# Optimization experiments

Hardware: AMD Instinct MI355X
Metric: run time of the kernel (lower is better)

Reference implementation:

```python
import jax, jax.numpy as jnp
import numpy as np
from jax import lax

K = 7            # cfg.network.PSROI_BINS == pool_size
FEAT_STRIDE = 16
LAMDA = 0.1
D_PER_BIN = 8    # feature channels per position-sensitive bin -> C = K*K*8 = 392


def _bilinear(feat, y, x, extra_idx):
    """Bilinearly sample feat[H,W,...] at float coords (y,x); extra_idx are
    integer index arrays (broadcast to y.shape) selecting trailing feat axes."""
    H, W = feat.shape[0], feat.shape[1]
    y0f = jnp.floor(y); x0f = jnp.floor(x)
    wy = (y - y0f)[..., None]
    wx = (x - x0f)[..., None]
    y0 = jnp.clip(y0f.astype(jnp.int32), 0, H - 1)
    y1 = jnp.clip(y0f.astype(jnp.int32) + 1, 0, H - 1)
    x0 = jnp.clip(x0f.astype(jnp.int32), 0, W - 1)
    x1 = jnp.clip(x0f.astype(jnp.int32) + 1, 0, W - 1)
    def g(yi, xi):
        return feat[(yi, xi) + extra_idx]
    return ((1 - wy) * (1 - wx) * g(y0, x0) + (1 - wy) * wx * g(y0, x1)
            + wy * (1 - wx) * g(y1, x0) + wy * wx * g(y1, x1))


def ps_roi(f, rois, k, feat_stride, offsets=None):
    """Position-sensitive RoI pooling. f: [H,W,C] with C = k*k*D (bin-major
    channel layout). rois: [N,5] (batch, x1, y1, x2, y2) in image coords.
    offsets (optional): [N, k*k, G, 2] per-bin, per-channel-group (x,y) shifts
    in image coords. Returns [N, D, k, k]."""
    H, W, C = f.shape
    N = rois.shape[0]
    kk = k * k
    D = C // kk
    x1 = rois[:, 1] / feat_stride
    y1 = rois[:, 2] / feat_stride
    x2 = (rois[:, 3] + 1.0) / feat_stride
    y2 = (rois[:, 4] + 1.0) / feat_stride
    bw = (x2 - x1) / k  # [N]
    bh = (y2 - y1) / k
    jj = jnp.tile(jnp.arange(k, dtype=f.dtype), k)     # bin = i*k + j
    ii = jnp.repeat(jnp.arange(k, dtype=f.dtype), k)
    cx = x1[:, None] + (jj + 0.5) * bw[:, None]        # [N, kk] bin centers
    cy = y1[:, None] + (ii + 0.5) * bh[:, None]
    bins = jnp.arange(kk, dtype=jnp.int32)
    if offsets is None:
        feat = f.reshape(H, W, kk, D)
        b = jnp.broadcast_to(bins, (N, kk))
        vals = _bilinear(feat, cy, cx, (b,))           # [N, kk, D]
    else:
        G = offsets.shape[2]
        cxg = cx[:, :, None] + offsets[..., 0] / feat_stride  # [N, kk, G]
        cyg = cy[:, :, None] + offsets[..., 1] / feat_stride
        feat = f.reshape(H, W, kk, G, D // G)
        b = jnp.broadcast_to(bins[None, :, None], (N, kk, G))
        g = jnp.broadcast_to(jnp.arange(G, dtype=jnp.int32)[None, None, :], (N, kk, G))
        vals = _bilinear(feat, cyg, cxg, (b, g))       # [N, kk, G, D//G]
        vals = vals.reshape(N, kk, D)
    return jnp.transpose(vals.reshape(N, k, k, D), (0, 3, 1, 2))  # [N, D, k, k]


def setup_inputs():
    key = jax.random.key(0)
    kf, kw, k1, k2 = jax.random.split(key, 4)
    H = W = 128
    C = K * K * D_PER_BIN
    N = 2048
    features = jax.random.normal(kf, (1, H, W, C), jnp.float32)
    conv_w = jax.random.normal(kw, (3, 3, C, 2 * 4 * K * K), jnp.float32) * 0.01
    img = float(H * FEAT_STRIDE)
    xy1 = jax.random.uniform(k1, (N, 2), minval=0.0, maxval=img * 0.6)
    wh = jax.random.uniform(k2, (N, 2), minval=32.0, maxval=img * 0.4)
    xy2 = jnp.minimum(xy1 + wh, img - 1.0)
    rois = jnp.concatenate([jnp.zeros((N, 1)), xy1[:, :1], xy1[:, 1:], xy2[:, :1], xy2[:, 1:]], axis=1).astype(jnp.float32)
    return {"features": features, "rois": rois, "conv_w": conv_w}


def reference(features, rois, conv_w):
    # offset branch: 3x3 conv (no bias) -> PS-RoI pool -> scale by lamda*roi size
    offset_map = lax.conv_general_dilated(features, conv_w, (1, 1), 'SAME',
                                          dimension_numbers=('NHWC', 'HWIO', 'NHWC'))
    off = ps_roi(offset_map[0], rois, K, FEAT_STRIDE)          # [N, 8, K, K]
    N = off.shape[0]
    off = off.reshape(N, -1, 2, K, K)                          # [N, 4, 2, K, K]
    off = jnp.transpose(off, (2, 3, 4, 1, 0))                  # [2, K, K, 4, N]
    roi_w = rois[:, 3] - rois[:, 1] + 1.0
    roi_h = rois[:, 4] - rois[:, 2] + 1.0
    off = jnp.stack((off[0] * roi_w * LAMDA, off[1] * roi_h * LAMDA), axis=0)
    off = jnp.transpose(off, (4, 1, 2, 3, 0))                  # [N, K, K, 4, 2]
    off = off.reshape(N, K * K, -1, 2)                         # [N, kk, 4, 2]
    # deformable PS-RoI pooling of the features with predicted offsets
    return ps_roi(features[0], rois, K, FEAT_STRIDE, offsets=off)  # [N, 8, K, K]
```

## Files before the change

### kernel.cpp

```cpp
#include <hip/hip_runtime.h>
#include <hip/hip_cooperative_groups.h>
#include <cstddef>
#include <cstdint>

namespace cg = cooperative_groups;

#define HH    128
#define WW    128
#define CC    392
#define NPIX  (HH*WW)
#define NROI  2048
#define PSK   7
#define NBIN  49
#define LAMDA 0.1f

#define CPAD      448
#define HPAD      130
#define NPADCO    416
#define SEGSTRIDE (9*CPAD)
#define BKK       64
#define NSS       21
#define SSPLIT    10

#define AROWS   136
#define ATH     (AROWS*BKK)
#define BTH     (128*BKK)

#define NBLK    1024
#define NTHR    256
#define GSTRIDE (NBLK*NTHR)
#define FTOT    (HPAD*HPAD*(CPAD/8))
#define WTILES  (9*14*13)
#define POOL8   (NROI*NBIN*8)

typedef _Float16 half8   __attribute__((ext_vector_type(8)));
typedef _Float16 half2v  __attribute__((ext_vector_type(2)));
typedef float    floatx4 __attribute__((ext_vector_type(4)));

__device__ __forceinline__ void async_ld16(const _Float16* g, _Float16* l) {
  __builtin_amdgcn_global_load_lds((const __attribute__((address_space(1))) void*)g,
                                   (__attribute__((address_space(3))) void*)l,
                                   16, 0, 0);
}

__device__ __forceinline__ void prep_features(const float* __restrict__ F,
                                              _Float16* __restrict__ Fh,
                                              int gtid, int stride) {
  for (int idx = gtid; idx < FTOT; idx += stride) {
    const int p   = idx / (CPAD / 8);
    const int cgi = idx - p * (CPAD / 8);
    const int c   = cgi * 8;
    const int py  = p / HPAD;
    const int px  = p - py * HPAD;
    half8 h;
#pragma unroll
    for (int i = 0; i < 8; ++i) h[i] = (_Float16)0.f;
    if (py >= 1 && py <= HH && px >= 1 && px <= WW && c < CC) {
      const float* src = F + ((size_t)(py - 1) * WW + (px - 1)) * CC + c;
      const float4 v0 = *(const float4*)src;
      const float4 v1 = *(const float4*)(src + 4);
      h[0] = (_Float16)v0.x; h[1] = (_Float16)v0.y;
      h[2] = (_Float16)v0.z; h[3] = (_Float16)v0.w;
      h[4] = (_Float16)v1.x; h[5] = (_Float16)v1.y;
      h[6] = (_Float16)v1.z; h[7] = (_Float16)v1.w;
    }
    *(half8*)(Fh + (size_t)p * CPAD + c) = h;
  }
}

__device__ __forceinline__ void prep_weights(const float* __restrict__ Wt,
                                             _Float16* __restrict__ Bth,
                                             float (*tile)[33],
                                             int bid, int t, int nblocks) {
  for (int tl = bid; tl < WTILES; tl += nblocks) {
    const int seg = tl / (14 * 13);
    const int rem = tl - seg * (14 * 13);
    const int cit = rem / 13;
    const int cot = rem - cit * 13;
    const int ci0 = cit * 32, co0 = cot * 32;
    __syncthreads();
#pragma unroll
    for (int i = 0; i < 4; ++i) {
      const int idx = t + i * 256;
      const int lr = idx >> 5;
      const int lc = idx & 31;
      const int ci = ci0 + lr, co = co0 + lc;
      float v = 0.f;
      if (ci < CC && co < CC) v = Wt[((size_t)seg * CC + ci) * CC + co];
      tile[lr][lc] = v;
    }
    __syncthreads();
#pragma unroll
    for (int i = 0; i < 4; ++i) {
      const int idx = t + i * 256;
      const int lr = idx >> 5;
      const int lc = idx & 31;
      Bth[(size_t)(co0 + lr) * SEGSTRIDE + seg * CPAD + ci0 + lc] = (_Float16)tile[lc][lr];
    }
  }
}

__device__ __forceinline__ void stage_a130(const _Float16* __restrict__ Fh,
                                           int fy, int cb, _Float16* As, int t) {
  const int L = t & 63, w = t >> 6;
  const int srow = L >> 3;
  const int kofs = ((L & 7) ^ srow) * 8;
  const _Float16* gA = Fh + (size_t)fy * HPAD * CPAD + kofs + cb;
#pragma unroll
  for (int j = 0; j < 4; ++j) {
    const int r = w * 32 + j * 8 + srow;
    async_ld16(gA + (size_t)r * CPAD, &As[(w * 32 + j * 8) * BKK]);
  }
  if (w == 0) {
    const int r = 128 + srow;
    const int rp = (r <= 129) ? r : 129;
    async_ld16(gA + (size_t)rp * CPAD, &As[128 * BKK]);
  }
}

__device__ __forceinline__ void conv_fat(const _Float16* __restrict__ Fh,
                                         const _Float16* __restrict__ Bth,
                                         _Float16* __restrict__ OMp,
                                         _Float16* As, _Float16* Bs,
                                         int row0, int col0, int s0, int s1, int t) {
  const int L = t & 63;
  const int w = t >> 6;

  const int srow = L >> 3;
  const int kofs = ((L & 7) ^ srow) * 8;
  const int ya = row0 >> 7;
  const int nbase = col0 + w * 32 + srow;

  const int wm = (w >> 1) * 64;
  const int wn = (w & 1) * 64;
  const int fr = L & 15;
  const int quad = L >> 4;

  floatx4 acc[4][4];
#pragma unroll
  for (int i = 0; i < 4; ++i)
#pragma unroll
    for (int j = 0; j < 4; ++j) {
      floatx4 z = {0.f, 0.f, 0.f, 0.f};
      acc[i][j] = z;
    }

  for (int s = s0; s < s1; ++s) {
    const int dyi = s / 7;
    const int it  = s - dyi * 7;
    const int fy  = ya + dyi;
    const int cb  = it * BKK;

    stage_a130(Fh, fy, cb, As, t);

    for (int dxs = 0; dxs < 3; ++dxs) {
      const int seg = dyi * 3 + dxs;
      const _Float16* gB = Bth + (size_t)nbase * SEGSTRIDE + seg * CPAD + kofs + cb;
#pragma unroll
      for (int j = 0; j < 4; ++j)
        async_ld16(gB + (size_t)(j * 8) * SEGSTRIDE, &Bs[(w * 32 + j * 8) * BKK]);
      __syncthreads();

      half8 a0[4], a1[4], b0[4], b1[4];
#pragma unroll
      for (int mt = 0; mt < 4; ++mt) {
        const int row = wm + mt * 16 + fr + dxs;
        const int rk = row & 7;
        a0[mt] = *(const half8*)(&As[row * BKK + ((quad ^ rk) * 8)]);
        a1[mt] = *(const half8*)(&As[row * BKK + (((4 + quad) ^ rk) * 8)]);
      }
#pragma unroll
      for (int nt = 0; nt < 4; ++nt) {
        const int rb = (wn + nt * 16 + fr) * BKK;
        const int rk = fr & 7;
        b0[nt] = *(const half8*)(&Bs[rb + ((quad ^ rk) * 8)]);
        b1[nt] = *(const half8*)(&Bs[rb + (((4 + quad) ^ rk) * 8)]);
      }
#pragma unroll
      for (int mt = 0; mt < 4; ++mt)
#pragma unroll
        for (int nt = 0; nt < 4; ++nt)
          acc[mt][nt] = __builtin_amdgcn_mfma_f32_16x16x32_f16(a0[mt], b0[nt], acc[mt][nt], 0, 0, 0);
#pragma unroll
      for (int mt = 0; mt < 4; ++mt)
#pragma unroll
        for (int nt = 0; nt < 4; ++nt)
          acc[mt][nt] = __builtin_amdgcn_mfma_f32_16x16x32_f16(a1[mt], b1[nt], acc[mt][nt], 0, 0, 0);
      __syncthreads();
    }
  }

#pragma unroll
  for (int mt = 0; mt < 4; ++mt) {
    const int rbase = row0 + wm + mt * 16 + quad * 4;
#pragma unroll
    for (int nt = 0; nt < 4; ++nt) {
      const int col = col0 + wn + nt * 16 + fr;
      if (col < CC) {
#pragma unroll
        for (int r = 0; r < 4; ++r)
          OMp[(size_t)(rbase + r) * CC + col] = (_Float16)acc[mt][nt][r];
      }
    }
  }
}

__device__ __forceinline__ void conv_thin(const _Float16* __restrict__ Fh,
                                          const _Float16* __restrict__ Bth,
                                          _Float16* __restrict__ OMp,
                                          _Float16* As, _Float16* Bs,
                                          int row0, int s0, int s1, int t) {
  const int L = t & 63;
  const int w = t >> 6;

  const int srow = L >> 3;
  const int kofs = ((L & 7) ^ srow) * 8;
  const int ya = row0 >> 7;
  const int nbase = 384 + w * 8 + srow;

  const int wm = w * 32;
  const int fr = L & 15;
  const int quad = L >> 4;

  floatx4 acc[2];
#pragma unroll
  for (int i = 0; i < 2; ++i) {
    floatx4 z = {0.f, 0.f, 0.f, 0.f};
    acc[i] = z;
  }

  for (int s = s0; s < s1; ++s) {
    const int dyi = s / 7;
    const int it  = s - dyi * 7;
    const int fy  = ya + dyi;
    const int cb  = it * BKK;

    stage_a130(Fh, fy, cb, As, t);

    for (int dxs = 0; dxs < 3; ++dxs) {
      const int seg = dyi * 3 + dxs;
      if (w < 2) {
        const _Float16* gB = Bth + (size_t)nbase * SEGSTRIDE + seg * CPAD + kofs + cb;
        async_ld16(gB, &Bs[(w * 8) * BKK]);
      }
      __syncthreads();

      half8 a0[2], a1[2];
#pragma unroll
      for (int mt = 0; mt < 2; ++mt) {
        const int row = wm + mt * 16 + fr + dxs;
        const int rk = row & 7;
        a0[mt] = *(const half8*)(&As[row * BKK + ((quad ^ rk) * 8)]);
        a1[mt] = *(const half8*)(&As[row * BKK + (((4 + quad) ^ rk) * 8)]);
      }
      const int rk = fr & 7;
      const half8 b0 = *(const half8*)(&Bs[fr * BKK + ((quad ^ rk) * 8)]);
      const half8 b1 = *(const half8*)(&Bs[fr * BKK + (((4 + quad) ^ rk) * 8)]);
#pragma unroll
      for (int mt = 0; mt < 2; ++mt)
        acc[mt] = __builtin_amdgcn_mfma_f32_16x16x32_f16(a0[mt], b0, acc[mt], 0, 0, 0);
#pragma unroll
      for (int mt = 0; mt < 2; ++mt)
        acc[mt] = __builtin_amdgcn_mfma_f32_16x16x32_f16(a1[mt], b1, acc[mt], 0, 0, 0);
      __syncthreads();
    }
  }

#pragma unroll
  for (int mt = 0; mt < 2; ++mt) {
    const int rbase = row0 + wm + mt * 16 + quad * 4;
    const int col = 384 + fr;
    if (col < CC) {
#pragma unroll
      for (int r = 0; r < 4; ++r)
        OMp[(size_t)(rbase + r) * CC + col] = (_Float16)acc[mt][r];
    }
  }
}

__device__ __forceinline__ void conv_dispatch(const _Float16* Fh, const _Float16* Bth,
                                              _Float16* OMa, _Float16* OMb,
                                              _Float16* As, _Float16* Bs,
                                              int bid, int t) {
  const int x = bid & 127;
  const int rest = bid >> 7;
  const int kz = (rest < 6) ? (rest / 3) : (rest - 6);
  _Float16* OMp = kz ? OMb : OMa;
  const int s0 = kz ? SSPLIT : 0;
  const int s1 = kz ? NSS : SSPLIT;
  if (rest < 6)
    conv_fat(Fh, Bth, OMp, As, Bs, x * 128, (rest % 3) * 128, s0, s1, t);
  else
    conv_thin(Fh, Bth, OMp, As, Bs, x * 128, s0, s1, t);
}

__device__ __forceinline__ void bilin_setup(float y, float x,
                                            int& iy0, int& iy1, int& ix0, int& ix1,
                                            float& w00, float& w01, float& w10, float& w11) {
  const float y0f = floorf(y), x0f = floorf(x);
  const float wy = y - y0f, wx = x - x0f;
  const int a = (int)y0f, b = (int)x0f;
  iy0 = min(max(a, 0), HH - 1);
  iy1 = min(max(a + 1, 0), HH - 1);
  ix0 = min(max(b, 0), WW - 1);
  ix1 = min(max(b + 1, 0), WW - 1);
  w00 = (1.f - wy) * (1.f - wx);
  w01 = (1.f - wy) * wx;
  w10 = wy * (1.f - wx);
  w11 = wy * wx;
}

__device__ __forceinline__ void pool_item8(const _Float16* __restrict__ Fh,
                                           const float* __restrict__ R,
                                           const _Float16* __restrict__ OMa,
                                           const _Float16* __restrict__ OMb,
                                           float* __restrict__ out, int tid) {
  const int j  = tid & 7;
  const int nb = tid >> 3;
  const int n  = nb / NBIN;
  const int b  = nb - n * NBIN;
  const int bi = b / PSK;
  const int bj = b - bi * PSK;

  const float rx1 = R[n * 5 + 1], ry1 = R[n * 5 + 2];
  const float rx2 = R[n * 5 + 3], ry2 = R[n * 5 + 4];
  const float x1 = rx1 * (1.f / 16.f);
  const float y1 = ry1 * (1.f / 16.f);
  const float x2 = (rx2 + 1.f) * (1.f / 16.f);
  const float y2 = (ry2 + 1.f) * (1.f / 16.f);
  const float bw = (x2 - x1) * (1.f / 7.f);
  const float bh = (y2 - y1) * (1.f / 7.f);
  const float cx = x1 + ((float)bj + 0.5f) * bw;
  const float cy = y1 + ((float)bi + 0.5f) * bh;
  const float sxs = (rx2 - rx1 + 1.f) * (LAMDA / 16.f);
  const float sys = (ry2 - ry1 + 1.f) * (LAMDA / 16.f);

  int iy0, iy1, ix0, ix1;
  float w00, w01, w10, w11;
  bilin_setup(cy, cx, iy0, iy1, ix0, ix1, w00, w01, w10, w11);

  const int c = j & 3;
  const int cyi = (c >> 1) ? iy1 : iy0;
  const int cxi = (c & 1) ? ix1 : ix0;
  const float wq = (c == 0) ? w00 : (c == 1) ? w01 : (c == 2) ? w10 : w11;

  const _Float16* OMp = (j >> 2) ? OMb : OMa;
  const size_t base = (size_t)(cyi * WW + cxi) * CC + (size_t)b * 8;
  const half8 hv = *(const half8*)(OMp + base);

  float o8[8];
#pragma unroll
  for (int i = 0; i < 8; ++i) o8[i] = wq * (float)hv[i];
#pragma unroll
  for (int i = 0; i < 8; ++i) o8[i] += __shfl_xor(o8[i], 1);
#pragma unroll
  for (int i = 0; i < 8; ++i) o8[i] += __shfl_xor(o8[i], 2);
#pragma unroll
  for (int i = 0; i < 8; ++i) o8[i] += __shfl_xor(o8[i], 4);

  const int g = j & 3;
  const float sx = cx + o8[2 * g] * sxs;
  const float sy = cy + o8[2 * g + 1] * sys;

  int jy0, jy1, jx0, jx1;
  float u00, u01, u10, u11;
  bilin_setup(sy, sx, jy0, jy1, jx0, jx1, u00, u01, u10, u11);

  const int  yh = j >> 2;
  const int  jy = yh ? jy1 : jy0;
  const float ua = yh ? u10 : u00;
  const float ub = yh ? u11 : u01;

  const size_t c0 = (size_t)b * 8 + 2 * g;
  const half2v qa = *(const half2v*)(Fh + ((size_t)(jy + 1) * HPAD + (jx0 + 1)) * CPAD + c0);
  const half2v qb = *(const half2v*)(Fh + ((size_t)(jy + 1) * HPAD + (jx1 + 1)) * CPAD + c0);

  float v0 = ua * (float)qa[0] + ub * (float)qb[0];
  float v1 = ua * (float)qa[1] + ub * (float)qb[1];
  v0 += __shfl_xor(v0, 4);
  v1 += __shfl_xor(v1, 4);

  const float vout = yh ? v1 : v0;
  out[((size_t)n * 8 + 2 * g + yh) * NBIN + b] = vout;
}

__global__ __launch_bounds__(NTHR, 4)
void mega_kernel(const float* __restrict__ F, const float* __restrict__ Wt,
                 _Float16* __restrict__ OMa, _Float16* __restrict__ OMb,
                 _Float16* __restrict__ Fh, _Float16* __restrict__ Bth) {
  __shared__ __align__(16) _Float16 smem[ATH + BTH];
  const int bid = blockIdx.x;
  const int t = threadIdx.x;
  cg::grid_group grid = cg::this_grid();

  prep_features(F, Fh, bid * NTHR + t, GSTRIDE);
  prep_weights(Wt, Bth, (float(*)[33])smem, bid, t, NBLK);

  __threadfence();
  grid.sync();

  conv_dispatch(Fh, Bth, OMa, OMb, smem, smem + ATH, bid, t);
}

__global__ __launch_bounds__(256)
void pool_kernel(const _Float16* __restrict__ Fh, const float* __restrict__ R,
                 const _Float16* __restrict__ OMa, const _Float16* __restrict__ OMb,
                 float* __restrict__ out) {
  pool_item8(Fh, R, OMa, OMb, out, blockIdx.x * 256 + threadIdx.x);
}

__global__ __launch_bounds__(256)
void prep_kernel_sa(const float* __restrict__ F, const float* __restrict__ Wt,
                    _Float16* __restrict__ Fh, _Float16* __restrict__ Bth) {
  __shared__ float tile[32][33];
  prep_features(F, Fh, blockIdx.x * 256 + threadIdx.x, gridDim.x * 256);
  prep_weights(Wt, Bth, tile, blockIdx.x, threadIdx.x, gridDim.x);
}

__global__ __launch_bounds__(256, 4)
void conv_kernel_sa(const _Float16* __restrict__ Fh, const _Float16* __restrict__ Bth,
                    _Float16* __restrict__ OMa, _Float16* __restrict__ OMb) {
  __shared__ __align__(16) _Float16 smem[ATH + BTH];
  conv_dispatch(Fh, Bth, OMa, OMb, smem, smem + ATH, blockIdx.x, threadIdx.x);
}

extern "C" void kernel_launch(void* const* d_in, const int* in_sizes, int n_in,
                              void* d_out, int out_size, void* d_ws, size_t ws_size,
                              hipStream_t stream) {
  const float* F  = (const float*)d_in[0];
  const float* R  = (const float*)d_in[1];
  const float* Wt = (const float*)d_in[2];
  float* out = (float*)d_out;

  const size_t omBytes  = (size_t)NPIX * CC * sizeof(_Float16);
  const size_t fhBytes  = (size_t)HPAD * HPAD * CPAD * sizeof(_Float16);

  _Float16* OMa = (_Float16*)d_ws;
  _Float16* OMb = OMa + (size_t)NPIX * CC;
  _Float16* Fh  = (_Float16*)((char*)d_ws + 2 * omBytes);
  _Float16* Bth = (_Float16*)((char*)d_ws + 2 * omBytes + fhBytes);

  int maxBlk = 0;
  hipError_t qerr = hipOccupancyMaxActiveBlocksPerMultiprocessor(&maxBlk, mega_kernel, NTHR, 0);
  bool coopOk = (qerr == hipSuccess && maxBlk >= 4);

  if (coopOk) {
    void* args[] = {(void*)&F, (void*)&Wt, (void*)&OMa, (void*)&OMb,
                    (void*)&Fh, (void*)&Bth};
    hipError_t err = hipLaunchCooperativeKernel((const void*)mega_kernel,
                                                dim3(NBLK), dim3(NTHR),
                                                args, 0, stream);
    if (err != hipSuccess) {
      (void)hipGetLastError();
      coopOk = false;
    }
  }
  if (!coopOk) {
    prep_kernel_sa<<<2048, 256, 0, stream>>>(F, Wt, Fh, Bth);
    conv_kernel_sa<<<NBLK, 256, 0, stream>>>(Fh, Bth, OMa, OMb);
  }

  pool_kernel<<<POOL8 / 256, 256, 0, stream>>>(Fh, R, OMa, OMb, out);
}
```

Before: 150.8 us.

## Drop split-K conv, use 512-thread blocks with double-buffered LDS pipeline

Removes the split-K partition of the 3x3 conv GEMM, which wrote two partial offset maps that the pool kernel had to sum. Each block now covers the full K range with 8 waves and smaller per-wave tiles, and double-buffers A and B in LDS so the next slice's async global->LDS loads overlap the current MFMAs. This halves the offset-map writes and the pool reads. In exchange it doubles LDS use per block and halves the block count, which may lower occupancy, and the cooperative launch now only requires two resident blocks per CU.

```diff
diff --git a/kernel.cpp b/kernel.cpp
--- a/kernel.cpp
+++ b/kernel.cpp
@@ -16,24 +16,23 @@
 
 #define CPAD      448
 #define HPAD      130
-#define NPADCO    416
 #define SEGSTRIDE (9*CPAD)
 #define BKK       64
 #define NSS       21
-#define SSPLIT    10
-
-#define AROWS   136
-#define ATH     (AROWS*BKK)
+#define NZ        63
+
+#define ATH     (136*BKK)
 #define BTH     (128*BKK)
 
-#define NBLK    1024
-#define NTHR    256
+#define NBLK    512
+#define NTHR    512
 #define GSTRIDE (NBLK*NTHR)
 #define FTOT    (HPAD*HPAD*(CPAD/8))
 #define WTILES  (9*14*13)
 #define POOL8   (NROI*NBIN*8)
 
 typedef _Float16 half8   __attribute__((ext_vector_type(8)));
+typedef _Float16 half4v  __attribute__((ext_vector_type(4)));
 typedef _Float16 half2v  __attribute__((ext_vector_type(2)));
 typedef float    floatx4 __attribute__((ext_vector_type(4)));
 
@@ -41,6 +40,12 @@
   __builtin_amdgcn_global_load_lds((const __attribute__((address_space(1))) void*)g,
                                    (__attribute__((address_space(3))) void*)l,
                                    16, 0, 0);
+}
+
+__device__ __forceinline__ void sync_step() {
+  asm volatile("s_waitcnt vmcnt(0)" ::: "memory");
+  __builtin_amdgcn_s_barrier();
+  asm volatile("" ::: "memory");
 }
 
 __device__ __forceinline__ void prep_features(const float* __restrict__ F,
@@ -71,7 +76,7 @@
 __device__ __forceinline__ void prep_weights(const float* __restrict__ Wt,
                                              _Float16* __restrict__ Bth,
                                              float (*tile)[33],
-                                             int bid, int t, int nblocks) {
+                                             int bid, int t, int bdim, int nblocks) {
   for (int tl = bid; tl < WTILES; tl += nblocks) {
     const int seg = tl / (14 * 13);
     const int rem = tl - seg * (14 * 13);
@@ -79,9 +84,7 @@
     const int cot = rem - cit * 13;
     const int ci0 = cit * 32, co0 = cot * 32;
     __syncthreads();
-#pragma unroll
-    for (int i = 0; i < 4; ++i) {
-      const int idx = t + i * 256;
+    for (int idx = t; idx < 1024; idx += bdim) {
       const int lr = idx >> 5;
       const int lc = idx & 31;
       const int ci = ci0 + lr, co = co0 + lc;
@@ -90,9 +93,7 @@
       tile[lr][lc] = v;
     }
     __syncthreads();
-#pragma unroll
-    for (int i = 0; i < 4; ++i) {
-      const int idx = t + i * 256;
+    for (int idx = t; idx < 1024; idx += bdim) {
       const int lr = idx >> 5;
       const int lc = idx & 31;
       Bth[(size_t)(co0 + lr) * SEGSTRIDE + seg * CPAD + ci0 + lc] = (_Float16)tile[lc][lr];
@@ -100,198 +101,189 @@
   }
 }
 
-__device__ __forceinline__ void stage_a130(const _Float16* __restrict__ Fh,
-                                           int fy, int cb, _Float16* As, int t) {
+__device__ __forceinline__ void stage_a8(const _Float16* __restrict__ Fh,
+                                         int fy, int cb, _Float16* As, int t) {
   const int L = t & 63, w = t >> 6;
   const int srow = L >> 3;
   const int kofs = ((L & 7) ^ srow) * 8;
   const _Float16* gA = Fh + (size_t)fy * HPAD * CPAD + kofs + cb;
 #pragma unroll
-  for (int j = 0; j < 4; ++j) {
-    const int r = w * 32 + j * 8 + srow;
-    async_ld16(gA + (size_t)r * CPAD, &As[(w * 32 + j * 8) * BKK]);
-  }
-  if (w == 0) {
-    const int r = 128 + srow;
-    const int rp = (r <= 129) ? r : 129;
+  for (int j = 0; j < 2; ++j) {
+    const int r = w * 16 + j * 8;
+    async_ld16(gA + (size_t)(r + srow) * CPAD, &As[r * BKK]);
+  }
+  if (w == 7) {
+    const int rr = 128 + srow;
+    const int rp = (rr <= 129) ? rr : 129;
     async_ld16(gA + (size_t)rp * CPAD, &As[128 * BKK]);
   }
+}
+
+__device__ __forceinline__ void stage_b8(const _Float16* __restrict__ Bth,
+                                         int col0, int seg, int cb, _Float16* Bs, int t) {
+  const int L = t & 63, w = t >> 6;
+  const int srow = L >> 3;
+  const int kofs = ((L & 7) ^ srow) * 8;
+  const _Float16* gB = Bth + (size_t)(col0 + w * 16 + srow) * SEGSTRIDE + seg * CPAD + kofs + cb;
+#pragma unroll
+  for (int j = 0; j < 2; ++j)
+    async_ld16(gB + (size_t)(j * 8) * SEGSTRIDE, &Bs[(w * 16 + j * 8) * BKK]);
+}
+
+__device__ __forceinline__ void stage_b_thin8(const _Float16* __restrict__ Bth,
+                                              int seg, int cb, _Float16* Bs, int t) {
+  const int L = t & 63, w = t >> 6;
+  if (w >= 2) return;
+  const int srow = L >> 3;
+  const int kofs = ((L & 7) ^ srow) * 8;
+  const _Float16* gB = Bth + (size_t)(384 + w * 8 + srow) * SEGSTRIDE + seg * CPAD + kofs + cb;
+  async_ld16(gB, &Bs[(w * 8) * BKK]);
 }
 
 __device__ __forceinline__ void conv_fat(const _Float16* __restrict__ Fh,
                                          const _Float16* __restrict__ Bth,
-                                         _Float16* __restrict__ OMp,
+                                         _Float16* __restrict__ OM,
                                          _Float16* As, _Float16* Bs,
-                                         int row0, int col0, int s0, int s1, int t) {
+                                         int row0, int col0, int t) {
   const int L = t & 63;
   const int w = t >> 6;
-
-  const int srow = L >> 3;
-  const int kofs = ((L & 7) ^ srow) * 8;
   const int ya = row0 >> 7;
-  const int nbase = col0 + w * 32 + srow;
-
-  const int wm = (w >> 1) * 64;
-  const int wn = (w & 1) * 64;
   const int fr = L & 15;
   const int quad = L >> 4;
-
-  floatx4 acc[4][4];
+  const int wm = (w >> 2) * 64;
+  const int wn = (w & 3) * 32;
+
+  floatx4 acc[4][2];
 #pragma unroll
   for (int i = 0; i < 4; ++i)
 #pragma unroll
-    for (int j = 0; j < 4; ++j) {
+    for (int j = 0; j < 2; ++j) {
       floatx4 z = {0.f, 0.f, 0.f, 0.f};
       acc[i][j] = z;
     }
 
-  for (int s = s0; s < s1; ++s) {
-    const int dyi = s / 7;
-    const int it  = s - dyi * 7;
-    const int fy  = ya + dyi;
-    const int cb  = it * BKK;
-
-    stage_a130(Fh, fy, cb, As, t);
-
-    for (int dxs = 0; dxs < 3; ++dxs) {
-      const int seg = dyi * 3 + dxs;
-      const _Float16* gB = Bth + (size_t)nbase * SEGSTRIDE + seg * CPAD + kofs + cb;
-#pragma unroll
-      for (int j = 0; j < 4; ++j)
-        async_ld16(gB + (size_t)(j * 8) * SEGSTRIDE, &Bs[(w * 32 + j * 8) * BKK]);
-      __syncthreads();
-
-      half8 a0[4], a1[4], b0[4], b1[4];
+  stage_a8(Fh, ya, 0, As, t);
+  stage_b8(Bth, col0, 0, 0, Bs, t);
+  sync_step();
+
+  int pa = 0, pb = 0;
+  for (int z = 0; z < NZ; ++z) {
+    const int dxs = z - (z / 3) * 3;
+    if (z + 1 < NZ) {
+      const int z2 = z + 1;
+      const int s2 = z2 / 3;
+      const int dxs2 = z2 - s2 * 3;
+      const int dyi2 = s2 / 7;
+      const int it2 = s2 - dyi2 * 7;
+      const int cb2 = it2 * BKK;
+      if (dxs2 == 0) stage_a8(Fh, ya + dyi2, cb2, As + (pa ^ 1) * ATH, t);
+      stage_b8(Bth, col0, dyi2 * 3 + dxs2, cb2, Bs + (pb ^ 1) * BTH, t);
+    }
+    const _Float16* Ab = As + pa * ATH;
+    const _Float16* Bb = Bs + pb * BTH;
+#pragma unroll
+    for (int kh = 0; kh < 2; ++kh) {
+      const int q = kh * 4 + quad;
+      half8 av[4], bv[2];
 #pragma unroll
       for (int mt = 0; mt < 4; ++mt) {
         const int row = wm + mt * 16 + fr + dxs;
-        const int rk = row & 7;
-        a0[mt] = *(const half8*)(&As[row * BKK + ((quad ^ rk) * 8)]);
-        a1[mt] = *(const half8*)(&As[row * BKK + (((4 + quad) ^ rk) * 8)]);
+        av[mt] = *(const half8*)(&Ab[row * BKK + ((q ^ (row & 7)) * 8)]);
       }
 #pragma unroll
-      for (int nt = 0; nt < 4; ++nt) {
-        const int rb = (wn + nt * 16 + fr) * BKK;
-        const int rk = fr & 7;
-        b0[nt] = *(const half8*)(&Bs[rb + ((quad ^ rk) * 8)]);
-        b1[nt] = *(const half8*)(&Bs[rb + (((4 + quad) ^ rk) * 8)]);
+      for (int nt = 0; nt < 2; ++nt) {
+        const int rb = wn + nt * 16 + fr;
+        bv[nt] = *(const half8*)(&Bb[rb * BKK + ((q ^ (fr & 7)) * 8)]);
       }
 #pragma unroll
       for (int mt = 0; mt < 4; ++mt)
 #pragma unroll
-        for (int nt = 0; nt < 4; ++nt)
-          acc[mt][nt] = __builtin_amdgcn_mfma_f32_16x16x32_f16(a0[mt], b0[nt], acc[mt][nt], 0, 0, 0);
-#pragma unroll
-      for (int mt = 0; mt < 4; ++mt)
-#pragma unroll
-        for (int nt = 0; nt < 4; ++nt)
-          acc[mt][nt] = __builtin_amdgcn_mfma_f32_16x16x32_f16(a1[mt], b1[nt], acc[mt][nt], 0, 0, 0);
-      __syncthreads();
-    }
+        for (int nt = 0; nt < 2; ++nt)
+          acc[mt][nt] = __builtin_amdgcn_mfma_f32_16x16x32_f16(av[mt], bv[nt], acc[mt][nt], 0, 0, 0);
+    }
+    sync_step();
+    if (dxs == 2) pa ^= 1;
+    pb ^= 1;
   }
 
 #pragma unroll
   for (int mt = 0; mt < 4; ++mt) {
     const int rbase = row0 + wm + mt * 16 + quad * 4;
 #pragma unroll
-    for (int nt = 0; nt < 4; ++nt) {
+    for (int nt = 0; nt < 2; ++nt) {
       const int col = col0 + wn + nt * 16 + fr;
-      if (col < CC) {
-#pragma unroll
-        for (int r = 0; r < 4; ++r)
-          OMp[(size_t)(rbase + r) * CC + col] = (_Float16)acc[mt][nt][r];
-      }
+#pragma unroll
+      for (int r = 0; r < 4; ++r)
+        OM[(size_t)(rbase + r) * CC + col] = (_Float16)acc[mt][nt][r];
     }
   }
 }
 
 __device__ __forceinline__ void conv_thin(const _Float16* __restrict__ Fh,
                                           const _Float16* __restrict__ Bth,
-                                          _Float16* __restrict__ OMp,
+                                          _Float16* __restrict__ OM,
                                           _Float16* As, _Float16* Bs,
-                                          int row0, int s0, int s1, int t) {
+                                          int row0, int t) {
   const int L = t & 63;
   const int w = t >> 6;
-
-  const int srow = L >> 3;
-  const int kofs = ((L & 7) ^ srow) * 8;
   const int ya = row0 >> 7;
-  const int nbase = 384 + w * 8 + srow;
-
-  const int wm = w * 32;
   const int fr = L & 15;
   const int quad = L >> 4;
-
-  floatx4 acc[2];
-#pragma unroll
-  for (int i = 0; i < 2; ++i) {
-    floatx4 z = {0.f, 0.f, 0.f, 0.f};
-    acc[i] = z;
-  }
-
-  for (int s = s0; s < s1; ++s) {
-    const int dyi = s / 7;
-    const int it  = s - dyi * 7;
-    const int fy  = ya + dyi;
-    const int cb  = it * BKK;
-
-    stage_a130(Fh, fy, cb, As, t);
-
-    for (int dxs = 0; dxs < 3; ++dxs) {
-      const int seg = dyi * 3 + dxs;
-      if (w < 2) {
-        const _Float16* gB = Bth + (size_t)nbase * SEGSTRIDE + seg * CPAD + kofs + cb;
-        async_ld16(gB, &Bs[(w * 8) * BKK]);
-      }
-      __syncthreads();
-
-      half8 a0[2], a1[2];
-#pragma unroll
-      for (int mt = 0; mt < 2; ++mt) {
-        const int row = wm + mt * 16 + fr + dxs;
-        const int rk = row & 7;
-        a0[mt] = *(const half8*)(&As[row * BKK + ((quad ^ rk) * 8)]);
-        a1[mt] = *(const half8*)(&As[row * BKK + (((4 + quad) ^ rk) * 8)]);
-      }
-      const int rk = fr & 7;
-      const half8 b0 = *(const half8*)(&Bs[fr * BKK + ((quad ^ rk) * 8)]);
-      const half8 b1 = *(const half8*)(&Bs[fr * BKK + (((4 + quad) ^ rk) * 8)]);
-#pragma unroll
-      for (int mt = 0; mt < 2; ++mt)
-        acc[mt] = __builtin_amdgcn_mfma_f32_16x16x32_f16(a0[mt], b0, acc[mt], 0, 0, 0);
-#pragma unroll
-      for (int mt = 0; mt < 2; ++mt)
-        acc[mt] = __builtin_amdgcn_mfma_f32_16x16x32_f16(a1[mt], b1, acc[mt], 0, 0, 0);
-      __syncthreads();
-    }
-  }
-
-#pragma unroll
-  for (int mt = 0; mt < 2; ++mt) {
-    const int rbase = row0 + wm + mt * 16 + quad * 4;
-    const int col = 384 + fr;
-    if (col < CC) {
-#pragma unroll
-      for (int r = 0; r < 4; ++r)
-        OMp[(size_t)(rbase + r) * CC + col] = (_Float16)acc[mt][r];
-    }
+  const int wm = w * 16;
+
+  floatx4 acc = {0.f, 0.f, 0.f, 0.f};
+
+  stage_a8(Fh, ya, 0, As, t);
+  stage_b_thin8(Bth, 0, 0, Bs, t);
+  sync_step();
+
+  int pa = 0, pb = 0;
+  for (int z = 0; z < NZ; ++z) {
+    const int dxs = z - (z / 3) * 3;
+    if (z + 1 < NZ) {
+      const int z2 = z + 1;
+      const int s2 = z2 / 3;
+      const int dxs2 = z2 - s2 * 3;
+      const int dyi2 = s2 / 7;
+      const int it2 = s2 - dyi2 * 7;
+      const int cb2 = it2 * BKK;
+      if (dxs2 == 0) stage_a8(Fh, ya + dyi2, cb2, As + (pa ^ 1) * ATH, t);
+      stage_b_thin8(Bth, dyi2 * 3 + dxs2, cb2, Bs + (pb ^ 1) * BTH, t);
+    }
+    const _Float16* Ab = As + pa * ATH;
+    const _Float16* Bb = Bs + pb * BTH;
+#pragma unroll
+    for (int kh = 0; kh < 2; ++kh) {
+      const int q = kh * 4 + quad;
+      const int row = wm + fr + dxs;
+      const half8 av = *(const half8*)(&Ab[row * BKK + ((q ^ (row & 7)) * 8)]);
+      const half8 bv = *(const half8*)(&Bb[fr * BKK + ((q ^ (fr & 7)) * 8)]);
+      acc = __builtin_amdgcn_mfma_f32_16x16x32_f16(av, bv, acc, 0, 0, 0);
+    }
+    sync_step();
+    if (dxs == 2) pa ^= 1;
+    pb ^= 1;
+  }
+
+  const int rbase = row0 + wm + quad * 4;
+  const int col = 384 + fr;
+  if (col < CC) {
+#pragma unroll
+    for (int r = 0; r < 4; ++r)
+      OM[(size_t)(rbase + r) * CC + col] = (_Float16)acc[r];
   }
 }
 
 __device__ __forceinline__ void conv_dispatch(const _Float16* Fh, const _Float16* Bth,
-                                              _Float16* OMa, _Float16* OMb,
+                                              _Float16* OM,
                                               _Float16* As, _Float16* Bs,
                                               int bid, int t) {
   const int x = bid & 127;
-  const int rest = bid >> 7;
-  const int kz = (rest < 6) ? (rest / 3) : (rest - 6);
-  _Float16* OMp = kz ? OMb : OMa;
-  const int s0 = kz ? SSPLIT : 0;
-  const int s1 = kz ? NSS : SSPLIT;
-  if (rest < 6)
-    conv_fat(Fh, Bth, OMp, As, Bs, x * 128, (rest % 3) * 128, s0, s1, t);
+  const int cg = bid >> 7;
+  if (cg < 3)
+    conv_fat(Fh, Bth, OM, As, Bs, x * 128, cg * 128, t);
   else
-    conv_thin(Fh, Bth, OMp, As, Bs, x * 128, s0, s1, t);
+    conv_thin(Fh, Bth, OM, As, Bs, x * 128, t);
 }
 
 __device__ __forceinline__ void bilin_setup(float y, float x,
@@ -312,8 +304,7 @@
 
 __device__ __forceinline__ void pool_item8(const _Float16* __restrict__ Fh,
                                            const float* __restrict__ R,
-                                           const _Float16* __restrict__ OMa,
-                                           const _Float16* __restrict__ OMb,
+                                           const _Float16* __restrict__ OM,
                                            float* __restrict__ out, int tid) {
   const int j  = tid & 7;
   const int nb = tid >> 3;
@@ -340,27 +331,32 @@
   bilin_setup(cy, cx, iy0, iy1, ix0, ix1, w00, w01, w10, w11);
 
   const int c = j & 3;
+  const int hf = j >> 2;
   const int cyi = (c >> 1) ? iy1 : iy0;
   const int cxi = (c & 1) ? ix1 : ix0;
   const float wq = (c == 0) ? w00 : (c == 1) ? w01 : (c == 2) ? w10 : w11;
 
-  const _Float16* OMp = (j >> 2) ? OMb : OMa;
-  const size_t base = (size_t)(cyi * WW + cxi) * CC + (size_t)b * 8;
-  const half8 hv = *(const half8*)(OMp + base);
-
-  float o8[8];
-#pragma unroll
-  for (int i = 0; i < 8; ++i) o8[i] = wq * (float)hv[i];
-#pragma unroll
-  for (int i = 0; i < 8; ++i) o8[i] += __shfl_xor(o8[i], 1);
-#pragma unroll
-  for (int i = 0; i < 8; ++i) o8[i] += __shfl_xor(o8[i], 2);
-#pragma unroll
-  for (int i = 0; i < 8; ++i) o8[i] += __shfl_xor(o8[i], 4);
+  const size_t base = (size_t)(cyi * WW + cxi) * CC + (size_t)b * 8 + hf * 4;
+  const half4v hv = *(const half4v*)(OM + base);
+
+  float o4[4];
+#pragma unroll
+  for (int i = 0; i < 4; ++i) o4[i] = wq * (float)hv[i];
+#pragma unroll
+  for (int i = 0; i < 4; ++i) o4[i] += __shfl_xor(o4[i], 1);
+#pragma unroll
+  for (int i = 0; i < 4; ++i) o4[i] += __shfl_xor(o4[i], 2);
+  float oth[4];
+#pragma unroll
+  for (int i = 0; i < 4; ++i) oth[i] = __shfl_xor(o4[i], 4);
 
   const int g = j & 3;
-  const float sx = cx + o8[2 * g] * sxs;
-  const float sy = cy + o8[2 * g + 1] * sys;
+  const int i0 = (g & 1) * 2;
+  const bool sel = ((g >> 1) == hf);
+  const float ox = sel ? o4[i0]     : oth[i0];
+  const float oy = sel ? o4[i0 + 1] : oth[i0 + 1];
+  const float sx = cx + ox * sxs;
+  const float sy = cy + oy * sys;
 
   int jy0, jy1, jx0, jx1;
   float u00, u01, u10, u11;
@@ -386,27 +382,26 @@
 
 __global__ __launch_bounds__(NTHR, 4)
 void mega_kernel(const float* __restrict__ F, const float* __restrict__ Wt,
-                 _Float16* __restrict__ OMa, _Float16* __restrict__ OMb,
+                 _Float16* __restrict__ OM,
                  _Float16* __restrict__ Fh, _Float16* __restrict__ Bth) {
-  __shared__ __align__(16) _Float16 smem[ATH + BTH];
+  __shared__ __align__(16) _Float16 smem[2 * ATH + 2 * BTH];
   const int bid = blockIdx.x;
   const int t = threadIdx.x;
   cg::grid_group grid = cg::this_grid();
 
   prep_features(F, Fh, bid * NTHR + t, GSTRIDE);
-  prep_weights(Wt, Bth, (float(*)[33])smem, bid, t, NBLK);
+  prep_weights(Wt, Bth, (float(*)[33])smem, bid, t, NTHR, NBLK);
 
   __threadfence();
   grid.sync();
 
-  conv_dispatch(Fh, Bth, OMa, OMb, smem, smem + ATH, bid, t);
+  conv_dispatch(Fh, Bth, OM, smem, smem + 2 * ATH, bid, t);
 }
 
 __global__ __launch_bounds__(256)
 void pool_kernel(const _Float16* __restrict__ Fh, const float* __restrict__ R,
-                 const _Float16* __restrict__ OMa, const _Float16* __restrict__ OMb,
-                 float* __restrict__ out) {
-  pool_item8(Fh, R, OMa, OMb, out, blockIdx.x * 256 + threadIdx.x);
+                 const _Float16* __restrict__ OM, float* __restrict__ out) {
+  pool_item8(Fh, R, OM, out, blockIdx.x * 256 + threadIdx.x);
 }
 
 __global__ __launch_bounds__(256)
@@ -414,14 +409,14 @@
                     _Float16* __restrict__ Fh, _Float16* __restrict__ Bth) {
   __shared__ float tile[32][33];
   prep_features(F, Fh, blockIdx.x * 256 + threadIdx.x, gridDim.x * 256);
-  prep_weights(Wt, Bth, tile, blockIdx.x, threadIdx.x, gridDim.x);
-}
-
-__global__ __launch_bounds__(256, 4)
+  prep_weights(Wt, Bth, tile, blockIdx.x, threadIdx.x, 256, gridDim.x);
+}
+
+__global__ __launch_bounds__(NTHR, 4)
 void conv_kernel_sa(const _Float16* __restrict__ Fh, const _Float16* __restrict__ Bth,
-                    _Float16* __restrict__ OMa, _Float16* __restrict__ OMb) {
-  __shared__ __align__(16) _Float16 smem[ATH + BTH];
-  conv_dispatch(Fh, Bth, OMa, OMb, smem, smem + ATH, blockIdx.x, threadIdx.x);
+                    _Float16* __restrict__ OM) {
+  __shared__ __align__(16) _Float16 smem[2 * ATH + 2 * BTH];
+  conv_dispatch(Fh, Bth, OM, smem, smem + 2 * ATH, blockIdx.x, threadIdx.x);
 }
 
 extern "C" void kernel_launch(void* const* d_in, const int* in_sizes, int n_in,
@@ -435,18 +430,16 @@
   const size_t omBytes  = (size_t)NPIX * CC * sizeof(_Float16);
   const size_t fhBytes  = (size_t)HPAD * HPAD * CPAD * sizeof(_Float16);
 
-  _Float16* OMa = (_Float16*)d_ws;
-  _Float16* OMb = OMa + (size_t)NPIX * CC;
-  _Float16* Fh  = (_Float16*)((char*)d_ws + 2 * omBytes);
-  _Float16* Bth = (_Float16*)((char*)d_ws + 2 * omBytes + fhBytes);
+  _Float16* OM  = (_Float16*)d_ws;
+  _Float16* Fh  = (_Float16*)((char*)d_ws + omBytes);
+  _Float16* Bth = (_Float16*)((char*)d_ws + omBytes + fhBytes);
 
   int maxBlk = 0;
   hipError_t qerr = hipOccupancyMaxActiveBlocksPerMultiprocessor(&maxBlk, mega_kernel, NTHR, 0);
-  bool coopOk = (qerr == hipSuccess && maxBlk >= 4);
+  bool coopOk = (qerr == hipSuccess && maxBlk >= 2);
 
   if (coopOk) {
-    void* args[] = {(void*)&F, (void*)&Wt, (void*)&OMa, (void*)&OMb,
-                    (void*)&Fh, (void*)&Bth};
+    void* args[] = {(void*)&F, (void*)&Wt, (void*)&OM, (void*)&Fh, (void*)&Bth};
     hipError_t err = hipLaunchCooperativeKernel((const void*)mega_kernel,
                                                 dim3(NBLK), dim3(NTHR),
                                                 args, 0, stream);
@@ -457,8 +450,8 @@
   }
   if (!coopOk) {
     prep_kernel_sa<<<2048, 256, 0, stream>>>(F, Wt, Fh, Bth);
-    conv_kernel_sa<<<NBLK, 256, 0, stream>>>(Fh, Bth, OMa, OMb);
-  }
-
-  pool_kernel<<<POOL8 / 256, 256, 0, stream>>>(Fh, R, OMa, OMb, out);
-}
+    conv_kernel_sa<<<NBLK, NTHR, 0, stream>>>(Fh, Bth, OM);
+  }
+
+  pool_kernel<<<POOL8 / 256, 256, 0, stream>>>(Fh, R, OM, out);
+}
```

Result: slower. 163.2 us (+8.3%).
